# Optimization experiments

Hardware: AMD Instinct MI355X
Metric: run time of the kernel (lower is better)

Reference implementation:

```python
import jax, jax.numpy as jnp
import numpy as np

D_MODEL = 1024
NUM_HEADS = 16
D_K = D_MODEL // NUM_HEADS
THETA = 10000.0
MAX_SEQ_LEN = 4096


def setup_inputs() -> dict:
    key = jax.random.key(0)
    ks = jax.random.split(key, 5)
    scale = 1.0 / np.sqrt(D_MODEL)
    x = jax.random.normal(ks[0], (2, 2048, D_MODEL), dtype=jnp.float32)
    wq = jax.random.normal(ks[1], (D_MODEL, D_MODEL), dtype=jnp.float32) * scale
    wk = jax.random.normal(ks[2], (D_MODEL, D_MODEL), dtype=jnp.float32) * scale
    wv = jax.random.normal(ks[3], (D_MODEL, D_MODEL), dtype=jnp.float32) * scale
    wo = jax.random.normal(ks[4], (D_MODEL, D_MODEL), dtype=jnp.float32) * scale
    return {"x": x, "wq": wq, "wk": wk, "wv": wv, "wo": wo}


def _rope(t, cos, sin):
    # t: (B, H, S, d_k) with interleaved even/odd pairs
    pairs = t.reshape(*t.shape[:-1], D_K // 2, 2)
    e, o = pairs[..., 0], pairs[..., 1]
    oe = e * cos - o * sin
    oo = e * sin + o * cos
    return jnp.stack([oe, oo], axis=-1).reshape(t.shape)


def reference(x, wq, wk, wv, wo):
    B, S, _ = x.shape
    # QKV projections (Linear: y = x @ W^T, no bias)
    def proj(w):
        y = jnp.einsum('bsd,ed->bse', x, w)
        return y.reshape(B, S, NUM_HEADS, D_K).transpose(0, 2, 1, 3)  # (B,H,S,dk)
    q, k, v = proj(wq), proj(wk), proj(wv)

    # RoPE angles for positions 0..S-1
    pair_idx = jnp.arange(0, D_K, 2, dtype=jnp.float32)
    inv_freq = 1.0 / (THETA ** (pair_idx / D_K))
    pos = jnp.arange(S, dtype=jnp.float32)
    ang = pos[:, None] * inv_freq[None, :]          # (S, dk/2)
    cos, sin = jnp.cos(ang), jnp.sin(ang)
    q = _rope(q, cos, sin)
    k = _rope(k, cos, sin)

    scores = jnp.einsum('bhqd,bhkd->bhqk', q, k) / jnp.sqrt(jnp.float32(D_K))
    causal = jnp.tril(jnp.ones((S, S), dtype=bool))
    scores = jnp.where(causal, scores, jnp.finfo(scores.dtype).min)
    attn = jax.nn.softmax(scores, axis=-1)
    out = jnp.einsum('bhqk,bhkd->bhqd', attn, v)    # (B,H,S,dk)
    out = out.transpose(0, 2, 1, 3).reshape(B, S, D_MODEL)
    return jnp.einsum('bsd,ed->bse', out, wo)
```

## Files before the change

kernel.cpp:

```cpp
#include <hip/hip_runtime.h>
#include <hip/hip_bf16.h>
#include <stdint.h>

#define S_LEN  2048
#define DMODEL 1024
#define NHEADS 16
#define DKH    64
#define NBATCH 2
#define NROWS  (NBATCH * S_LEN)
#define NBH    (NBATCH * NHEADS)
#define KVS    72
#define HB     (128 * 32)

typedef unsigned short ushort_t;
typedef __attribute__((ext_vector_type(8))) short bf16x8;
typedef __attribute__((ext_vector_type(4))) short bf16x4;
typedef __attribute__((ext_vector_type(4))) float f32x4;
typedef __attribute__((ext_vector_type(4))) unsigned short us4;

__device__ __forceinline__ ushort_t f2bf(float f) {
  union { float f; unsigned int u; } c; c.f = f;
  unsigned int r = c.u + 0x7FFFu + ((c.u >> 16) & 1u);
  return (ushort_t)(r >> 16);
}

__device__ __forceinline__ unsigned int pack_bf16(float lo, float hi) {
  union { __hip_bfloat162 h; unsigned int u; } cv;
  cv.h = __float22bfloat162_rn(make_float2(lo, hi));
  return cv.u;
}

__device__ __forceinline__ f32x4 mfma16(bf16x4 a, bf16x4 b, f32x4 c) {
#if __has_builtin(__builtin_amdgcn_mfma_f32_16x16x16_bf16)
  return __builtin_amdgcn_mfma_f32_16x16x16_bf16(a, b, c, 0, 0, 0);
#elif __has_builtin(__builtin_amdgcn_mfma_f32_16x16x16bf16_1k)
  return __builtin_amdgcn_mfma_f32_16x16x16bf16_1k(a, b, c, 0, 0, 0);
#else
  asm volatile("v_mfma_f32_16x16x16_bf16 %0, %1, %2, %0" : "+v"(c) : "v"(a), "v"(b));
  return c;
#endif
}

__device__ __forceinline__ void gload_lds16(const void* g, void* l) {
  __builtin_amdgcn_global_load_lds((const __attribute__((address_space(1))) void*)g,
                                   (__attribute__((address_space(3))) void*)l, 16, 0, 0);
}

__global__ void cast5_kernel(const float* __restrict__ x,
                             const float* __restrict__ a, const float* __restrict__ b,
                             const float* __restrict__ c, const float* __restrict__ d,
                             ushort_t* __restrict__ dst) {
  const int i = (blockIdx.x * 256 + threadIdx.x) * 4;
  const int sel = i >> 20;
  const float* src;
  int off;
  if (sel < 4)      { src = x; off = i; }
  else if (sel == 4){ src = a; off = i & ((1 << 20) - 1); }
  else if (sel == 5){ src = b; off = i & ((1 << 20) - 1); }
  else if (sel == 6){ src = c; off = i & ((1 << 20) - 1); }
  else              { src = d; off = i & ((1 << 20) - 1); }
  const float4 v = *(const float4*)(src + off);
  us4 o;
  o.x = f2bf(v.x); o.y = f2bf(v.y); o.z = f2bf(v.z); o.w = f2bf(v.w);
  *(us4*)(dst + i) = o;
}

template<int EPI>
__device__ __forceinline__ void gemm_core(const ushort_t* __restrict__ A, const ushort_t* __restrict__ Bm,
                                          void* __restrict__ Cp, void* __restrict__ Cp2,
                                          int N, int r0, int c0,
                                          ushort_t* As, ushort_t* Bs)
{
  const int tid  = threadIdx.x;
  const int lane = tid & 63;
  const int w    = tid >> 6;
  const int wr   = (w >> 1) * 64;
  const int wc   = (w & 1) * 64;
  const int g    = lane >> 4;
  const int lr   = lane & 15;
  const int K    = 1024;

  f32x4 acc[4][4] = {};

  const int idx0 = tid, idx1 = 256 + tid;
  const int row0 = idx0 >> 2, ce0 = (idx0 & 3) * 8;
  const int row1 = idx1 >> 2, ce1 = (idx1 & 3) * 8;

  for (int k0 = 0; k0 < K; k0 += 64) {
    #pragma unroll
    for (int hh = 0; hh < 2; hh++) {
      const int kk = k0 + hh * 32;
      ushort_t* Ah = As + hh * HB;
      ushort_t* Bh = Bs + hh * HB;
      gload_lds16(A  + (size_t)(r0 + row0) * K + kk + ce0, Ah + idx0 * 8);
      gload_lds16(A  + (size_t)(r0 + row1) * K + kk + ce1, Ah + idx1 * 8);
      gload_lds16(Bm + (size_t)(c0 + row0) * K + kk + ce0, Bh + idx0 * 8);
      gload_lds16(Bm + (size_t)(c0 + row1) * K + kk + ce1, Bh + idx1 * 8);
    }
    __syncthreads();
    #pragma unroll
    for (int hh = 0; hh < 2; hh++) {
      const ushort_t* Ah = As + hh * HB;
      const ushort_t* Bh = Bs + hh * HB;
      bf16x8 af[4], bfr[4];
      #pragma unroll
      for (int i = 0; i < 4; i++) {
        af[i]  = *(const bf16x8*)(Ah + (wr + i * 16 + lr) * 32 + g * 8);
        bfr[i] = *(const bf16x8*)(Bh + (wc + i * 16 + lr) * 32 + g * 8);
      }
      #pragma unroll
      for (int mf = 0; mf < 4; mf++)
        #pragma unroll
        for (int nf = 0; nf < 4; nf++)
          acc[mf][nf] = __builtin_amdgcn_mfma_f32_16x16x32_bf16(af[mf], bfr[nf], acc[mf][nf], 0, 0, 0);
    }
    __syncthreads();
  }

  #pragma unroll
  for (int mf = 0; mf < 4; mf++) {
    #pragma unroll
    for (int nf = 0; nf < 4; nf++) {
      #pragma unroll
      for (int r = 0; r < 4; r++) {
        const int row = r0 + wr + mf * 16 + g * 4 + r;
        const int col = c0 + wc + nf * 16 + lr;
        float v = acc[mf][nf][r];
        if constexpr (EPI == 0) {
          ((ushort_t*)Cp)[(size_t)row * N + col] = f2bf(v);
        } else {
          float pv = __shfl_xor(v, 1);
          const int cc  = col & (DMODEL - 1);
          const int pos = row & (S_LEN - 1);
          const int d   = cc & (DKH - 1);
          const int pr  = d >> 1;
          const float inv = exp2f((float)pr * -0.41524100952f);
          const float ang = (float)pos * inv;
          float sn, cs;
          __sincosf(ang, &sn, &cs);
          float outv = (d & 1) ? (pv * sn + v * cs) : (v * cs - pv * sn);
          if (col < DMODEL) outv *= 0.18033688011f;
          const int b = row >> 11, s = row & (S_LEN - 1);
          const int h = cc >> 6;
          ushort_t* dst = (ushort_t*)((col < DMODEL) ? Cp : Cp2);
          dst[(((size_t)(b * NHEADS + h)) * S_LEN + s) * DKH + d] = f2bf(outv);
        }
      }
    }
  }
}

__global__ __launch_bounds__(256, 3)
void proj_kernel(const ushort_t* __restrict__ xb, const ushort_t* __restrict__ wqb,
                 const ushort_t* __restrict__ wvb,
                 ushort_t* __restrict__ qb, ushort_t* __restrict__ kb, ushort_t* __restrict__ vtb)
{
  __shared__ ushort_t As[2 * HB];
  __shared__ ushort_t Bs[2 * HB];
  const int lin = (int)blockIdx.x;
  const int nl  = (lin & 7) * 96 + (lin >> 3);
  if (nl < 512) {
    gemm_core<2>(xb, wqb, qb, kb, 2 * DMODEL, (nl >> 4) * 128, (nl & 15) * 128, As, Bs);
  } else {
    const int m = nl - 512;
    gemm_core<0>(wvb, xb, vtb, nullptr, NROWS, (m >> 5) * 128, (m & 31) * 128, As, Bs);
  }
}

__global__ __launch_bounds__(256, 2)
void gemm_final(const ushort_t* __restrict__ A, const ushort_t* __restrict__ Bm,
                float* __restrict__ Cp)
{
  __shared__ ushort_t As[128 * 32];
  __shared__ ushort_t Bs[64 * 32];
  const int lin  = (int)blockIdx.x;
  const int nl   = (lin & 7) * 64 + (lin >> 3);
  const int r0   = (nl >> 4) * 128;
  const int c0   = (nl & 15) * 64;
  const int tid  = threadIdx.x;
  const int lane = tid & 63;
  const int w    = tid >> 6;
  const int wr   = (w >> 1) * 64;
  const int wc   = (w & 1) * 32;
  const int g    = lane >> 4;
  const int lr   = lane & 15;
  const int K    = 1024;

  f32x4 acc[4][2] = {};
  const int idx0 = tid, idx1 = 256 + tid;
  const int rowA0 = idx0 >> 2, ceA0 = (idx0 & 3) * 8;
  const int rowA1 = idx1 >> 2, ceA1 = (idx1 & 3) * 8;
  const int rowB  = tid >> 2,  ceB  = (tid & 3) * 8;

  for (int k0 = 0; k0 < K; k0 += 32) {
    gload_lds16(A  + (size_t)(r0 + rowA0) * K + k0 + ceA0, As + idx0 * 8);
    gload_lds16(A  + (size_t)(r0 + rowA1) * K + k0 + ceA1, As + idx1 * 8);
    gload_lds16(Bm + (size_t)(c0 + rowB) * K + k0 + ceB,  Bs + tid * 8);
    __syncthreads();
    bf16x8 af[4], bfr[2];
    #pragma unroll
    for (int i = 0; i < 4; i++)
      af[i] = *(const bf16x8*)(As + (wr + i * 16 + lr) * 32 + g * 8);
    #pragma unroll
    for (int i = 0; i < 2; i++)
      bfr[i] = *(const bf16x8*)(Bs + (wc + i * 16 + lr) * 32 + g * 8);
    #pragma unroll
    for (int mf = 0; mf < 4; mf++)
      #pragma unroll
      for (int nf = 0; nf < 2; nf++)
        acc[mf][nf] = __builtin_amdgcn_mfma_f32_16x16x32_bf16(af[mf], bfr[nf], acc[mf][nf], 0, 0, 0);
    __syncthreads();
  }
  #pragma unroll
  for (int mf = 0; mf < 4; mf++)
    #pragma unroll
    for (int nf = 0; nf < 2; nf++)
      #pragma unroll
      for (int r = 0; r < 4; r++) {
        const int row = r0 + wr + mf * 16 + g * 4 + r;
        const int col = c0 + wc + nf * 16 + lr;
        Cp[(size_t)row * DMODEL + col] = acc[mf][nf][r];
      }
}

__global__ __launch_bounds__(512, 4)
void attn_kernel(const ushort_t* __restrict__ Q, const ushort_t* __restrict__ Kh,
                 const ushort_t* __restrict__ VT, ushort_t* __restrict__ Out)
{
  __shared__ ushort_t Ks[2][64 * KVS];
  __shared__ ushort_t Vs[2][64 * KVS];
  const int tid  = threadIdx.x;
  const int lane = tid & 63;
  const int w    = tid >> 6;
  const int grp  = w >> 2;
  const int wid  = w & 3;
  const int g    = lane >> 4, lr = lane & 15;

  const int id = (int)blockIdx.x;
  const int bh = id & 31;
  const int qt = 31 - (id >> 5);
  const int b  = bh >> 4, h = bh & 15;

  const ushort_t* Kbase = Kh + (size_t)bh * S_LEN * DKH;
  const ushort_t* Vbase = VT + (size_t)h * DKH * (size_t)NROWS + (size_t)b * S_LEN;

  ushort_t* Ksg = &Ks[grp][0];
  ushort_t* Vsg = &Vs[grp][0];
  float* MB = (float*)&Ks[1][0];
  float* SB = MB + 64 * 68;

  const int tg   = tid & 255;
  const int krow = tg >> 3;
  const int kcol = (tg & 7) * 8;

  const int qrow = qt * 64 + wid * 16;

  bf16x8 qf0, qf1;
  {
    const ushort_t* qp = Q + ((size_t)bh * S_LEN + qrow + lr) * DKH;
    qf0 = *(const bf16x8*)(qp + g * 8);
    qf1 = *(const bf16x8*)(qp + 32 + g * 8);
  }
  f32x4 o[4] = {};
  float lsum = 0.f;

  bf16x8 kr0, kr1, vr0, vr1;
  if (grp <= qt) {
    const int kv0 = grp * 64;
    kr0 = *(const bf16x8*)(Kbase + (size_t)(kv0 + krow) * DKH + kcol);
    kr1 = *(const bf16x8*)(Kbase + (size_t)(kv0 + 32 + krow) * DKH + kcol);
    vr0 = *(const bf16x8*)(Vbase + (size_t)krow * NROWS + kv0 + kcol);
    vr1 = *(const bf16x8*)(Vbase + (size_t)(32 + krow) * NROWS + kv0 + kcol);
  }

  const int nT = qt / 2 + 1;
  for (int t = 0; t < nT; t++) {
    const int tk  = 2 * t + grp;
    const bool act = (tk <= qt);
    const bool pre = (tk + 2 <= qt);

    __syncthreads();
    if (act) {
      *(bf16x8*)(Ksg + krow * KVS + kcol) = kr0;
      *(bf16x8*)(Ksg + (32 + krow) * KVS + kcol) = kr1;
      *(bf16x8*)(Vsg + krow * KVS + kcol) = vr0;
      *(bf16x8*)(Vsg + (32 + krow) * KVS + kcol) = vr1;
    }
    __syncthreads();
    if (pre) {
      const int kv0n = (tk + 2) * 64;
      kr0 = *(const bf16x8*)(Kbase + (size_t)(kv0n + krow) * DKH + kcol);
      kr1 = *(const bf16x8*)(Kbase + (size_t)(kv0n + 32 + krow) * DKH + kcol);
      vr0 = *(const bf16x8*)(Vbase + (size_t)krow * NROWS + kv0n + kcol);
      vr1 = *(const bf16x8*)(Vbase + (size_t)(32 + krow) * NROWS + kv0n + kcol);
    }

    if (act) {
      f32x4 s4[4];
      __builtin_amdgcn_s_setprio(1);
      #pragma unroll
      for (int nf = 0; nf < 4; nf++) {
        bf16x8 b0 = *(const bf16x8*)(Ksg + (nf * 16 + lr) * KVS + g * 8);
        bf16x8 b1 = *(const bf16x8*)(Ksg + (nf * 16 + lr) * KVS + 32 + g * 8);
        f32x4 z = {};
        z = __builtin_amdgcn_mfma_f32_16x16x32_bf16(b0, qf0, z, 0, 0, 0);
        z = __builtin_amdgcn_mfma_f32_16x16x32_bf16(b1, qf1, z, 0, 0, 0);
        s4[nf] = z;
      }
      __builtin_amdgcn_s_setprio(0);

      if (tk == qt) {
        const int qg = qrow + lr;
        #pragma unroll
        for (int nf = 0; nf < 4; nf++) {
          const int kvb = tk * 64 + nf * 16 + g * 4;
          #pragma unroll
          for (int r = 0; r < 4; r++)
            if (kvb + r > qg) s4[nf][r] = -3.0e38f;
        }
      }

      float p[4][4];
      #pragma unroll
      for (int nf = 0; nf < 4; nf++)
        #pragma unroll
        for (int r = 0; r < 4; r++) p[nf][r] = __builtin_amdgcn_exp2f(s4[nf][r]);
      lsum += ((p[0][0] + p[0][1]) + (p[0][2] + p[0][3])) + ((p[1][0] + p[1][1]) + (p[1][2] + p[1][3]))
            + ((p[2][0] + p[2][1]) + (p[2][2] + p[2][3])) + ((p[3][0] + p[3][1]) + (p[3][2] + p[3][3]));

      bf16x4 pf[4];
      #pragma unroll
      for (int nfk = 0; nfk < 4; nfk++) {
        union { unsigned int u[2]; bf16x4 v; } cv;
        cv.u[0] = pack_bf16(p[nfk][0], p[nfk][1]);
        cv.u[1] = pack_bf16(p[nfk][2], p[nfk][3]);
        pf[nfk] = cv.v;
      }

      __builtin_amdgcn_s_setprio(1);
      #pragma unroll
      for (int nfk = 0; nfk < 4; nfk++)
        #pragma unroll
        for (int nfo = 0; nfo < 4; nfo++) {
          const bf16x4 vB = *(const bf16x4*)(Vsg + (nfo * 16 + lr) * KVS + nfk * 16 + g * 4);
          o[nfo] = mfma16(pf[nfk], vB, o[nfo]);
        }
      __builtin_amdgcn_s_setprio(0);
    }
  }

  lsum += __shfl_xor(lsum, 16);
  lsum += __shfl_xor(lsum, 32);

  __syncthreads();
  if (grp == 1) {
    #pragma unroll
    for (int nf = 0; nf < 4; nf++)
      #pragma unroll
      for (int r = 0; r < 4; r++)
        MB[(wid * 16 + g * 4 + r) * 68 + nf * 16 + lr] = o[nf][r];
    if (g == 0) SB[wid * 16 + lr] = lsum;
  }
  __syncthreads();
  if (grp == 0) {
    #pragma unroll
    for (int r = 0; r < 4; r++) {
      const int rl  = g * 4 + r;
      const int rho = wid * 16 + rl;
      const float lB = SB[rho];
      const float lA = __shfl(lsum, (lane & 48) | rl);
      const float inv = 1.0f / (lA + lB);
      const int s = qt * 64 + rho;
      #pragma unroll
      for (int nf = 0; nf < 4; nf++) {
        const float val = (o[nf][r] + MB[rho * 68 + nf * 16 + lr]) * inv;
        Out[((size_t)b * S_LEN + s) * DMODEL + h * DKH + nf * 16 + lr] = f2bf(val);
      }
    }
  }
}

extern "C" void kernel_launch(void* const* d_in, const int* in_sizes, int n_in,
                              void* d_out, int out_size, void* d_ws, size_t ws_size,
                              hipStream_t stream)
{
  const float* x  = (const float*)d_in[0];
  const float* wq = (const float*)d_in[1];
  const float* wk = (const float*)d_in[2];
  const float* wv = (const float*)d_in[3];
  const float* wo = (const float*)d_in[4];
  float* out = (float*)d_out;
  ushort_t* ws = (ushort_t*)d_ws;

  ushort_t* xb  = ws;
  ushort_t* wqb = xb  + (size_t)NROWS * DMODEL;
  ushort_t* wkb = wqb + (size_t)DMODEL * DMODEL;
  ushort_t* wvb = wkb + (size_t)DMODEL * DMODEL;
  ushort_t* wob = wvb + (size_t)DMODEL * DMODEL;
  ushort_t* qb  = wob + (size_t)DMODEL * DMODEL;
  ushort_t* kb  = qb  + (size_t)NROWS * DMODEL;
  ushort_t* vtb = kb  + (size_t)NROWS * DMODEL;
  ushort_t* ab  = xb;

  cast5_kernel<<<8192, 256, 0, stream>>>(x, wq, wk, wv, wo, ws);

  proj_kernel<<<768, 256, 0, stream>>>(xb, wqb, wvb, qb, kb, vtb);
  attn_kernel<<<1024, 512, 0, stream>>>(qb, kb, vtb, ab);
  gemm_final<<<512, 256, 0, stream>>>(ab, wob, out);
}
```

Before: 101.9 us.

## Drop intra-block KV split in attention; use single 4-wave group per query tile

The attention kernel previously ran two 4-wave groups per block that processed alternating KV tiles and then merged partial outputs and row sums through shared memory. It now uses 256-thread blocks in which every wave walks all KV tiles sequentially, with a single shared K/V buffer and no cross-group merge. This removes the merge step, its extra syncs and half the LDS, and raises the launch-bounds target for occupancy. In exchange each block has a longer serial KV loop, with less parallelism per query tile, which can hurt the long causal tiles.

```diff
diff --git a/kernel.cpp b/kernel.cpp
--- a/kernel.cpp
+++ b/kernel.cpp
@@ -223,17 +223,15 @@
       }
 }
 
-__global__ __launch_bounds__(512, 4)
+__global__ __launch_bounds__(256, 8)
 void attn_kernel(const ushort_t* __restrict__ Q, const ushort_t* __restrict__ Kh,
                  const ushort_t* __restrict__ VT, ushort_t* __restrict__ Out)
 {
-  __shared__ ushort_t Ks[2][64 * KVS];
-  __shared__ ushort_t Vs[2][64 * KVS];
+  __shared__ ushort_t Ks[64 * KVS];
+  __shared__ ushort_t Vs[64 * KVS];
   const int tid  = threadIdx.x;
   const int lane = tid & 63;
-  const int w    = tid >> 6;
-  const int grp  = w >> 2;
-  const int wid  = w & 3;
+  const int wid  = tid >> 6;
   const int g    = lane >> 4, lr = lane & 15;
 
   const int id = (int)blockIdx.x;
@@ -244,14 +242,8 @@
   const ushort_t* Kbase = Kh + (size_t)bh * S_LEN * DKH;
   const ushort_t* Vbase = VT + (size_t)h * DKH * (size_t)NROWS + (size_t)b * S_LEN;
 
-  ushort_t* Ksg = &Ks[grp][0];
-  ushort_t* Vsg = &Vs[grp][0];
-  float* MB = (float*)&Ks[1][0];
-  float* SB = MB + 64 * 68;
-
-  const int tg   = tid & 255;
-  const int krow = tg >> 3;
-  const int kcol = (tg & 7) * 8;
+  const int krow = tid >> 3;
+  const int kcol = (tid & 7) * 8;
 
   const int qrow = qt * 64 + wid * 16;
 
@@ -265,118 +257,87 @@
   float lsum = 0.f;
 
   bf16x8 kr0, kr1, vr0, vr1;
-  if (grp <= qt) {
-    const int kv0 = grp * 64;
-    kr0 = *(const bf16x8*)(Kbase + (size_t)(kv0 + krow) * DKH + kcol);
-    kr1 = *(const bf16x8*)(Kbase + (size_t)(kv0 + 32 + krow) * DKH + kcol);
-    vr0 = *(const bf16x8*)(Vbase + (size_t)krow * NROWS + kv0 + kcol);
-    vr1 = *(const bf16x8*)(Vbase + (size_t)(32 + krow) * NROWS + kv0 + kcol);
-  }
-
-  const int nT = qt / 2 + 1;
-  for (int t = 0; t < nT; t++) {
-    const int tk  = 2 * t + grp;
-    const bool act = (tk <= qt);
-    const bool pre = (tk + 2 <= qt);
-
-    __syncthreads();
-    if (act) {
-      *(bf16x8*)(Ksg + krow * KVS + kcol) = kr0;
-      *(bf16x8*)(Ksg + (32 + krow) * KVS + kcol) = kr1;
-      *(bf16x8*)(Vsg + krow * KVS + kcol) = vr0;
-      *(bf16x8*)(Vsg + (32 + krow) * KVS + kcol) = vr1;
-    }
-    __syncthreads();
-    if (pre) {
-      const int kv0n = (tk + 2) * 64;
+  kr0 = *(const bf16x8*)(Kbase + (size_t)krow * DKH + kcol);
+  kr1 = *(const bf16x8*)(Kbase + (size_t)(32 + krow) * DKH + kcol);
+  vr0 = *(const bf16x8*)(Vbase + (size_t)krow * NROWS + kcol);
+  vr1 = *(const bf16x8*)(Vbase + (size_t)(32 + krow) * NROWS + kcol);
+
+  for (int tk = 0; tk <= qt; tk++) {
+    __syncthreads();
+    *(bf16x8*)(Ks + krow * KVS + kcol) = kr0;
+    *(bf16x8*)(Ks + (32 + krow) * KVS + kcol) = kr1;
+    *(bf16x8*)(Vs + krow * KVS + kcol) = vr0;
+    *(bf16x8*)(Vs + (32 + krow) * KVS + kcol) = vr1;
+    __syncthreads();
+    if (tk < qt) {
+      const int kv0n = (tk + 1) * 64;
       kr0 = *(const bf16x8*)(Kbase + (size_t)(kv0n + krow) * DKH + kcol);
       kr1 = *(const bf16x8*)(Kbase + (size_t)(kv0n + 32 + krow) * DKH + kcol);
       vr0 = *(const bf16x8*)(Vbase + (size_t)krow * NROWS + kv0n + kcol);
       vr1 = *(const bf16x8*)(Vbase + (size_t)(32 + krow) * NROWS + kv0n + kcol);
     }
 
-    if (act) {
-      f32x4 s4[4];
-      __builtin_amdgcn_s_setprio(1);
+    f32x4 s4[4];
+    __builtin_amdgcn_s_setprio(1);
+    #pragma unroll
+    for (int nf = 0; nf < 4; nf++) {
+      bf16x8 b0 = *(const bf16x8*)(Ks + (nf * 16 + lr) * KVS + g * 8);
+      bf16x8 b1 = *(const bf16x8*)(Ks + (nf * 16 + lr) * KVS + 32 + g * 8);
+      f32x4 z = {};
+      z = __builtin_amdgcn_mfma_f32_16x16x32_bf16(b0, qf0, z, 0, 0, 0);
+      z = __builtin_amdgcn_mfma_f32_16x16x32_bf16(b1, qf1, z, 0, 0, 0);
+      s4[nf] = z;
+    }
+    __builtin_amdgcn_s_setprio(0);
+
+    if (tk == qt) {
+      const int qg = qrow + lr;
       #pragma unroll
       for (int nf = 0; nf < 4; nf++) {
-        bf16x8 b0 = *(const bf16x8*)(Ksg + (nf * 16 + lr) * KVS + g * 8);
-        bf16x8 b1 = *(const bf16x8*)(Ksg + (nf * 16 + lr) * KVS + 32 + g * 8);
-        f32x4 z = {};
-        z = __builtin_amdgcn_mfma_f32_16x16x32_bf16(b0, qf0, z, 0, 0, 0);
-        z = __builtin_amdgcn_mfma_f32_16x16x32_bf16(b1, qf1, z, 0, 0, 0);
-        s4[nf] = z;
-      }
-      __builtin_amdgcn_s_setprio(0);
-
-      if (tk == qt) {
-        const int qg = qrow + lr;
+        const int kvb = tk * 64 + nf * 16 + g * 4;
         #pragma unroll
-        for (int nf = 0; nf < 4; nf++) {
-          const int kvb = tk * 64 + nf * 16 + g * 4;
-          #pragma unroll
-          for (int r = 0; r < 4; r++)
-            if (kvb + r > qg) s4[nf][r] = -3.0e38f;
-        }
-      }
-
-      float p[4][4];
-      #pragma unroll
-      for (int nf = 0; nf < 4; nf++)
-        #pragma unroll
-        for (int r = 0; r < 4; r++) p[nf][r] = __builtin_amdgcn_exp2f(s4[nf][r]);
-      lsum += ((p[0][0] + p[0][1]) + (p[0][2] + p[0][3])) + ((p[1][0] + p[1][1]) + (p[1][2] + p[1][3]))
-            + ((p[2][0] + p[2][1]) + (p[2][2] + p[2][3])) + ((p[3][0] + p[3][1]) + (p[3][2] + p[3][3]));
-
-      bf16x4 pf[4];
-      #pragma unroll
-      for (int nfk = 0; nfk < 4; nfk++) {
-        union { unsigned int u[2]; bf16x4 v; } cv;
-        cv.u[0] = pack_bf16(p[nfk][0], p[nfk][1]);
-        cv.u[1] = pack_bf16(p[nfk][2], p[nfk][3]);
-        pf[nfk] = cv.v;
-      }
-
-      __builtin_amdgcn_s_setprio(1);
-      #pragma unroll
-      for (int nfk = 0; nfk < 4; nfk++)
-        #pragma unroll
-        for (int nfo = 0; nfo < 4; nfo++) {
-          const bf16x4 vB = *(const bf16x4*)(Vsg + (nfo * 16 + lr) * KVS + nfk * 16 + g * 4);
-          o[nfo] = mfma16(pf[nfk], vB, o[nfo]);
-        }
-      __builtin_amdgcn_s_setprio(0);
-    }
+        for (int r = 0; r < 4; r++)
+          if (kvb + r > qg) s4[nf][r] = -3.0e38f;
+      }
+    }
+
+    float p[4][4];
+    #pragma unroll
+    for (int nf = 0; nf < 4; nf++)
+      #pragma unroll
+      for (int r = 0; r < 4; r++) p[nf][r] = __builtin_amdgcn_exp2f(s4[nf][r]);
+    lsum += ((p[0][0] + p[0][1]) + (p[0][2] + p[0][3])) + ((p[1][0] + p[1][1]) + (p[1][2] + p[1][3]))
+          + ((p[2][0] + p[2][1]) + (p[2][2] + p[2][3])) + ((p[3][0] + p[3][1]) + (p[3][2] + p[3][3]));
+
+    bf16x4 pf[4];
+    #pragma unroll
+    for (int nfk = 0; nfk < 4; nfk++) {
+      union { unsigned int u[2]; bf16x4 v; } cv;
+      cv.u[0] = pack_bf16(p[nfk][0], p[nfk][1]);
+      cv.u[1] = pack_bf16(p[nfk][2], p[nfk][3]);
+      pf[nfk] = cv.v;
+    }
+
+    __builtin_amdgcn_s_setprio(1);
+    #pragma unroll
+    for (int nfk = 0; nfk < 4; nfk++)
+      #pragma unroll
+      for (int nfo = 0; nfo < 4; nfo++) {
+        const bf16x4 vB = *(const bf16x4*)(Vs + (nfo * 16 + lr) * KVS + nfk * 16 + g * 4);
+        o[nfo] = mfma16(pf[nfk], vB, o[nfo]);
+      }
+    __builtin_amdgcn_s_setprio(0);
   }
 
   lsum += __shfl_xor(lsum, 16);
   lsum += __shfl_xor(lsum, 32);
-
-  __syncthreads();
-  if (grp == 1) {
+  #pragma unroll
+  for (int r = 0; r < 4; r++) {
+    const float invr = 1.0f / __shfl(lsum, (lane & 48) | (g * 4 + r));
+    const int s = qrow + g * 4 + r;
     #pragma unroll
     for (int nf = 0; nf < 4; nf++)
-      #pragma unroll
-      for (int r = 0; r < 4; r++)
-        MB[(wid * 16 + g * 4 + r) * 68 + nf * 16 + lr] = o[nf][r];
-    if (g == 0) SB[wid * 16 + lr] = lsum;
-  }
-  __syncthreads();
-  if (grp == 0) {
-    #pragma unroll
-    for (int r = 0; r < 4; r++) {
-      const int rl  = g * 4 + r;
-      const int rho = wid * 16 + rl;
-      const float lB = SB[rho];
-      const float lA = __shfl(lsum, (lane & 48) | rl);
-      const float inv = 1.0f / (lA + lB);
-      const int s = qt * 64 + rho;
-      #pragma unroll
-      for (int nf = 0; nf < 4; nf++) {
-        const float val = (o[nf][r] + MB[rho * 68 + nf * 16 + lr]) * inv;
-        Out[((size_t)b * S_LEN + s) * DMODEL + h * DKH + nf * 16 + lr] = f2bf(val);
-      }
-    }
+      Out[((size_t)b * S_LEN + s) * DMODEL + h * DKH + nf * 16 + lr] = f2bf(o[nf][r] * invr);
   }
 }
 
@@ -405,6 +366,6 @@
   cast5_kernel<<<8192, 256, 0, stream>>>(x, wq, wk, wv, wo, ws);
 
   proj_kernel<<<768, 256, 0, stream>>>(xb, wqb, wvb, qb, kb, vtb);
-  attn_kernel<<<1024, 512, 0, stream>>>(qb, kb, vtb, ab);
+  attn_kernel<<<1024, 256, 0, stream>>>(qb, kb, vtb, ab);
   gemm_final<<<512, 256, 0, stream>>>(ab, wob, out);
 }
```

After: 143.1 us. +40.5%, slower.
